# Kernel tuning notes

Hardware: AMD Instinct MI355X
Metric: run time of the kernel (lower is better)

Reference implementation:

```python
import jax, jax.numpy as jnp
import numpy as np
from jax import lax

T = 4          # num_steps
TAU = 2.0      # spikingjelly LIFNode default tau
VTH = 1.0      # v_threshold
ALPHA = 2.0    # ATan surrogate default alpha
EPS = 1e-5     # BatchNorm eps

@jax.custom_vjp
def atan_spike(x):
    # Heaviside forward, ATan surrogate backward (spikingjelly surrogate.ATan)
    return (x >= 0.0).astype(x.dtype)

def _atan_fwd(x):
    return atan_spike(x), x

def _atan_bwd(x, g):
    sg = (ALPHA / 2.0) / (1.0 + (jnp.pi / 2.0 * ALPHA * x) ** 2)
    return (g * sg,)

atan_spike.defvjp(_atan_fwd, _atan_bwd)

def lif_multistep(x_seq):
    # x_seq: (T, B, D, L). LIF with decay_input=True, v_reset=0.0, hard reset,
    # detach_reset=True (reset spike is stop-gradiented).
    def step(v, xt):
        h = v + (xt - v) / TAU          # membrane charge
        s = atan_spike(h - VTH)          # spike
        v_new = h * (1.0 - lax.stop_gradient(s))  # hard reset to 0
        return v_new, s
    _, spikes = lax.scan(step, jnp.zeros_like(x_seq[0]), x_seq)
    return spikes  # (T, B, D, L)

def setup_inputs() -> dict:
    key = jax.random.key(0)
    k1, k2, k3, k4 = jax.random.split(key, 4)
    L, TB, D = 2048, 128, 128
    x = jax.random.normal(k1, (L, TB, D), dtype=jnp.float32)
    conv_w = jax.random.normal(k2, (D, D, 3), dtype=jnp.float32) * 0.05
    bn_gamma = jnp.ones((D,), jnp.float32)
    bn_beta = jnp.zeros((D,), jnp.float32)
    bn_mean = jax.random.normal(k3, (D,), dtype=jnp.float32) * 0.1
    bn_var = jax.random.uniform(k4, (D,), dtype=jnp.float32, minval=0.5, maxval=1.5)
    return {"x": x, "conv_w": conv_w, "bn_gamma": bn_gamma, "bn_beta": bn_beta,
            "bn_mean": bn_mean, "bn_var": bn_var}

def reference(x, conv_w, bn_gamma, bn_beta, bn_mean, bn_var):
    # x: (L, TB, D)
    L, TB, D = x.shape
    xf = jnp.transpose(x, (1, 2, 0))  # (TB, D, L)
    # Conv1d(D, D, k=3, stride=1, pad=1, bias=False)
    xf = lax.conv_general_dilated(xf, conv_w, window_strides=(1,),
                                  padding=((1, 1),),
                                  dimension_numbers=("NCH", "OIH", "NCH"))
    # BatchNorm1d in inference mode (running stats)
    scale = bn_gamma * lax.rsqrt(bn_var + EPS)
    xf = (xf - bn_mean[None, :, None]) * scale[None, :, None] + bn_beta[None, :, None]
    # (TB, D, L) -> (T, B, D, L), multi-step LIF
    xs = xf.reshape(T, TB // T, D, L)
    sp = lif_multistep(xs)
    sp = sp.reshape(TB, D, L)   # flatten(0, 1); dropout is identity in eval
    return x + jnp.transpose(sp, (2, 0, 1))  # (L, TB, D)
```

## Files before the change

### kernel.cpp

```cpp
#include <hip/hip_runtime.h>


constexpr int L   = 2048;
constexpr int NTB = 128;
constexpr int D   = 128;
constexpr int T   = 4;
constexpr int LT  = 64;
constexpr int NP  = LT + 2;
constexpr int JT  = 16;
constexpr int IT  = 8;
constexpr int WROW = 52;

__global__ __launch_bounds__(256, 3)
void snn_conv_lif(const float* __restrict__ x, const float* __restrict__ w,
                  const float* __restrict__ gamma, const float* __restrict__ beta,
                  const float* __restrict__ mean, const float* __restrict__ var,
                  float* __restrict__ out) {
    __shared__ float xs[NP * D];
    __shared__ float ws[64 * WROW];

    const int tid = threadIdx.x;
    const int b   = blockIdx.x & 31;
    const int lt  = blockIdx.x >> 5;
    const int l0  = lt * LT;
    const int q   = tid & 63;
    const int lh  = tid >> 6;
    const int p0  = lh * JT;

    const int o0 = 2 * q, o1 = o0 + 1;
    const float sc0 = gamma[o0] / sqrtf(var[o0] + 1e-5f);
    const float bi0 = beta[o0] - mean[o0] * sc0;
    const float sc1 = gamma[o1] / sqrtf(var[o1] + 1e-5f);
    const float bi1 = beta[o1] - mean[o1] * sc1;

    float v0[JT], v1[JT];
    #pragma unroll
    for (int j = 0; j < JT; ++j) { v0[j] = 0.f; v1[j] = 0.f; }

    #pragma unroll 1
    for (int t = 0; t < T; ++t) {
        const int n = t * 32 + b;
        __syncthreads();
        for (int idx = tid; idx < NP * 32; idx += 256) {
            const int p = idx >> 5, c = idx & 31;
            const int l = l0 - 1 + p;
            float4 val = make_float4(0.f, 0.f, 0.f, 0.f);
            if (l >= 0 && l < L)
                val = ((const float4*)x)[l * (NTB * D / 4) + n * (D / 4) + c];
            ((float4*)xs)[p * (D / 4) + c] = val;
        }

        float a0[JT], a1[JT];
        #pragma unroll
        for (int j = 0; j < JT; ++j) { a0[j] = 0.f; a1[j] = 0.f; }

        #pragma unroll 1
        for (int it = 0; it < D / IT; ++it) {
            __syncthreads();
            for (int idx = tid; idx < 768; idx += 256) {
                const int qq = idx / 12;
                const int r  = idx - qq * 12;
                const int oo = (r >= 6) ? 1 : 0;
                const int c  = r - 6 * oo;
                float4 wv = ((const float4*)(w + (2 * qq + oo) * (D * 3) + it * (IT * 3)))[c];
                *((float4*)(ws + qq * WROW + oo * 28 + c * 4)) = wv;
            }
            __syncthreads();

            const float* wrow = ws + q * WROW;
            #pragma unroll
            for (int i4 = 0; i4 < IT / 4; ++i4) {
                const float4 wa0 = *((const float4*)(wrow + i4 * 12));
                const float4 wa1 = *((const float4*)(wrow + i4 * 12 + 4));
                const float4 wa2 = *((const float4*)(wrow + i4 * 12 + 8));
                const float4 wb0 = *((const float4*)(wrow + 28 + i4 * 12));
                const float4 wb1 = *((const float4*)(wrow + 28 + i4 * 12 + 4));
                const float4 wb2 = *((const float4*)(wrow + 28 + i4 * 12 + 8));
                const float wA[12] = {wa0.x, wa0.y, wa0.z, wa0.w,
                                      wa1.x, wa1.y, wa1.z, wa1.w,
                                      wa2.x, wa2.y, wa2.z, wa2.w};
                const float wB[12] = {wb0.x, wb0.y, wb0.z, wb0.w,
                                      wb1.x, wb1.y, wb1.z, wb1.w,
                                      wb2.x, wb2.y, wb2.z, wb2.w};
                const float4* xcol = (const float4*)xs + (it * 2 + i4);
                float4 xa = xcol[(p0 + 0) * (D / 4)];
                float4 xb = xcol[(p0 + 1) * (D / 4)];
                #pragma unroll
                for (int j = 0; j < JT; ++j) {
                    const float4 xc = xcol[(p0 + j + 2) * (D / 4)];
                    float s0 = a0[j];
                    float s1 = a1[j];
                    s0 = fmaf(xa.x, wA[0], s0);   s1 = fmaf(xa.x, wB[0], s1);
                    s0 = fmaf(xa.y, wA[3], s0);   s1 = fmaf(xa.y, wB[3], s1);
                    s0 = fmaf(xa.z, wA[6], s0);   s1 = fmaf(xa.z, wB[6], s1);
                    s0 = fmaf(xa.w, wA[9], s0);   s1 = fmaf(xa.w, wB[9], s1);
                    s0 = fmaf(xb.x, wA[1], s0);   s1 = fmaf(xb.x, wB[1], s1);
                    s0 = fmaf(xb.y, wA[4], s0);   s1 = fmaf(xb.y, wB[4], s1);
                    s0 = fmaf(xb.z, wA[7], s0);   s1 = fmaf(xb.z, wB[7], s1);
                    s0 = fmaf(xb.w, wA[10], s0);  s1 = fmaf(xb.w, wB[10], s1);
                    s0 = fmaf(xc.x, wA[2], s0);   s1 = fmaf(xc.x, wB[2], s1);
                    s0 = fmaf(xc.y, wA[5], s0);   s1 = fmaf(xc.y, wB[5], s1);
                    s0 = fmaf(xc.z, wA[8], s0);   s1 = fmaf(xc.z, wB[8], s1);
                    s0 = fmaf(xc.w, wA[11], s0);  s1 = fmaf(xc.w, wB[11], s1);
                    a0[j] = s0; a1[j] = s1;
                    xa = xb; xb = xc;
                }
            }
        }

        #pragma unroll
        for (int j = 0; j < JT; ++j) {
            const float y0 = fmaf(a0[j], sc0, bi0);
            const float y1 = fmaf(a1[j], sc1, bi1);
            const float h0 = 0.5f * (v0[j] + y0);
            const float h1 = 0.5f * (v1[j] + y1);
            const bool f0 = (h0 >= 1.0f);
            const bool f1 = (h1 >= 1.0f);
            v0[j] = f0 ? 0.0f : h0;
            v1[j] = f1 ? 0.0f : h1;
            const int l = l0 + p0 + j;
            const float2 res = ((const float2*)xs)[(p0 + j + 1) * (D / 2) + q];
            float2 ov;
            ov.x = res.x + (f0 ? 1.0f : 0.0f);
            ov.y = res.y + (f1 ? 1.0f : 0.0f);
            ((float2*)out)[(l * NTB + n) * (D / 2) + q] = ov;
        }
    }
}

extern "C" void kernel_launch(void* const* d_in, const int* in_sizes, int n_in,
                              void* d_out, int out_size, void* d_ws, size_t ws_size,
                              hipStream_t stream) {
    const float* x     = (const float*)d_in[0];
    const float* w     = (const float*)d_in[1];
    const float* gamma = (const float*)d_in[2];
    const float* beta  = (const float*)d_in[3];
    const float* mean  = (const float*)d_in[4];
    const float* var   = (const float*)d_in[5];
    float* out = (float*)d_out;

    dim3 grid((L / LT) * 32);
    dim3 block(256);
    snn_conv_lif<<<grid, block, 0, stream>>>(x, w, gamma, beta, mean, var, out);
}
```

Measured before the change: 623.2 us.

## Read conv inputs directly from global and double-buffer weight tiles in LDS

Drops the shared-memory staging of the input tile. Each wave now loads its x values straight from global memory as wave-uniform broadcast loads, since lh is made uniform with readfirstlane. Weight chunks are double-buffered in LDS, with the next chunk prefetched into registers while the current one is used, so each inner iteration needs one barrier instead of two. The trade-off is many more global/L1 loads for x in place of LDS reads, and it relies on scalar or broadcast loads being cheap.

```diff
diff --git a/kernel.cpp b/kernel.cpp
--- a/kernel.cpp
+++ b/kernel.cpp
@@ -6,32 +6,50 @@
 constexpr int D   = 128;
 constexpr int T   = 4;
 constexpr int LT  = 64;
-constexpr int NP  = LT + 2;
 constexpr int JT  = 16;
 constexpr int IT  = 8;
 constexpr int WROW = 52;
+
+__device__ __forceinline__ float4 ldx(const float* __restrict__ x, int l, int n, int cb) {
+    const int lc = (l < 0) ? 0 : ((l >= L) ? (L - 1) : l);
+    float4 v = ((const float4*)x)[(lc * NTB + n) * (D / 4) + cb];
+    if (l < 0 || l >= L) v = make_float4(0.f, 0.f, 0.f, 0.f);
+    return v;
+}
 
 __global__ __launch_bounds__(256, 3)
 void snn_conv_lif(const float* __restrict__ x, const float* __restrict__ w,
                   const float* __restrict__ gamma, const float* __restrict__ beta,
                   const float* __restrict__ mean, const float* __restrict__ var,
                   float* __restrict__ out) {
-    __shared__ float xs[NP * D];
-    __shared__ float ws[64 * WROW];
+    __shared__ float ws[2][64 * WROW];
 
     const int tid = threadIdx.x;
     const int b   = blockIdx.x & 31;
     const int lt  = blockIdx.x >> 5;
     const int l0  = lt * LT;
     const int q   = tid & 63;
-    const int lh  = tid >> 6;
+    const int lh  = __builtin_amdgcn_readfirstlane(tid >> 6);
     const int p0  = lh * JT;
+    const int lb  = l0 - 1 + p0;
 
     const int o0 = 2 * q, o1 = o0 + 1;
     const float sc0 = gamma[o0] / sqrtf(var[o0] + 1e-5f);
     const float bi0 = beta[o0] - mean[o0] * sc0;
     const float sc1 = gamma[o1] / sqrtf(var[o1] + 1e-5f);
     const float bi1 = beta[o1] - mean[o1] * sc1;
+
+    const int qq = tid >> 2;
+    const int r3 = 3 * (tid & 3);
+    int grow[3], lrow[3];
+    #pragma unroll
+    for (int c = 0; c < 3; ++c) {
+        const int rr = r3 + c;
+        const int oo = (rr >= 6) ? 1 : 0;
+        const int c6 = rr - 6 * oo;
+        grow[c] = (2 * qq + oo) * (D * 3) + c6 * 4;
+        lrow[c] = qq * WROW + oo * 28 + c6 * 4;
+    }
 
     float v0[JT], v1[JT];
     #pragma unroll
@@ -40,15 +58,13 @@
     #pragma unroll 1
     for (int t = 0; t < T; ++t) {
         const int n = t * 32 + b;
+
+        #pragma unroll
+        for (int c = 0; c < 3; ++c) {
+            const float4 wv = *((const float4*)(w + grow[c]));
+            *((float4*)(&ws[0][lrow[c]])) = wv;
+        }
         __syncthreads();
-        for (int idx = tid; idx < NP * 32; idx += 256) {
-            const int p = idx >> 5, c = idx & 31;
-            const int l = l0 - 1 + p;
-            float4 val = make_float4(0.f, 0.f, 0.f, 0.f);
-            if (l >= 0 && l < L)
-                val = ((const float4*)x)[l * (NTB * D / 4) + n * (D / 4) + c];
-            ((float4*)xs)[p * (D / 4) + c] = val;
-        }
 
         float a0[JT], a1[JT];
         #pragma unroll
@@ -56,18 +72,16 @@
 
         #pragma unroll 1
         for (int it = 0; it < D / IT; ++it) {
-            __syncthreads();
-            for (int idx = tid; idx < 768; idx += 256) {
-                const int qq = idx / 12;
-                const int r  = idx - qq * 12;
-                const int oo = (r >= 6) ? 1 : 0;
-                const int c  = r - 6 * oo;
-                float4 wv = ((const float4*)(w + (2 * qq + oo) * (D * 3) + it * (IT * 3)))[c];
-                *((float4*)(ws + qq * WROW + oo * 28 + c * 4)) = wv;
+            const int cur = it & 1;
+
+            float4 wp[3];
+            if (it < 15) {
+                #pragma unroll
+                for (int c = 0; c < 3; ++c)
+                    wp[c] = *((const float4*)(w + grow[c] + (it + 1) * (IT * 3)));
             }
-            __syncthreads();
 
-            const float* wrow = ws + q * WROW;
+            const float* wrow = &ws[cur][q * WROW];
             #pragma unroll
             for (int i4 = 0; i4 < IT / 4; ++i4) {
                 const float4 wa0 = *((const float4*)(wrow + i4 * 12));
@@ -82,12 +96,13 @@
                 const float wB[12] = {wb0.x, wb0.y, wb0.z, wb0.w,
                                       wb1.x, wb1.y, wb1.z, wb1.w,
                                       wb2.x, wb2.y, wb2.z, wb2.w};
-                const float4* xcol = (const float4*)xs + (it * 2 + i4);
-                float4 xa = xcol[(p0 + 0) * (D / 4)];
-                float4 xb = xcol[(p0 + 1) * (D / 4)];
+
+                const int cb = it * 2 + i4;
+                float4 xa = ldx(x, lb + 0, n, cb);
+                float4 xb = ldx(x, lb + 1, n, cb);
                 #pragma unroll
                 for (int j = 0; j < JT; ++j) {
-                    const float4 xc = xcol[(p0 + j + 2) * (D / 4)];
+                    const float4 xc = ldx(x, lb + j + 2, n, cb);
                     float s0 = a0[j];
                     float s1 = a1[j];
                     s0 = fmaf(xa.x, wA[0], s0);   s1 = fmaf(xa.x, wB[0], s1);
@@ -106,6 +121,13 @@
                     xa = xb; xb = xc;
                 }
             }
+
+            if (it < 15) {
+                #pragma unroll
+                for (int c = 0; c < 3; ++c)
+                    *((float4*)(&ws[cur ^ 1][lrow[c]])) = wp[c];
+            }
+            __syncthreads();
         }
 
         #pragma unroll
@@ -119,7 +141,7 @@
             v0[j] = f0 ? 0.0f : h0;
             v1[j] = f1 ? 0.0f : h1;
             const int l = l0 + p0 + j;
-            const float2 res = ((const float2*)xs)[(p0 + j + 1) * (D / 2) + q];
+            const float2 res = ((const float2*)x)[(l * NTB + n) * (D / 2) + q];
             float2 ov;
             ov.x = res.x + (f0 ? 1.0f : 0.0f);
             ov.y = res.y + (f1 ? 1.0f : 0.0f);
```

Result: slower. 1.844 ms (+195.8%).

## Load conv weights directly from global into registers with software prefetch

Applied to the files above, without the earlier changes.

Drops the shared-memory weight staging and its two barriers per 8-channel chunk. Each thread now reads its two output channels' weight rows straight from global memory (L1/L2 cached) into registers, prefetching the next 4-channel group while computing the current one. This removes LDS traffic and the frequent __syncthreads. The cost is more vector registers and uncoalesced global loads, since each lane reads a different 1.5KB row.

```diff
diff --git a/kernel.cpp b/kernel.cpp
--- a/kernel.cpp
+++ b/kernel.cpp
@@ -8,8 +8,6 @@
 constexpr int LT  = 64;
 constexpr int NP  = LT + 2;
 constexpr int JT  = 16;
-constexpr int IT  = 8;
-constexpr int WROW = 52;
 
 __global__ __launch_bounds__(256, 3)
 void snn_conv_lif(const float* __restrict__ x, const float* __restrict__ w,
@@ -17,7 +15,6 @@
                   const float* __restrict__ mean, const float* __restrict__ var,
                   float* __restrict__ out) {
     __shared__ float xs[NP * D];
-    __shared__ float ws[64 * WROW];
 
     const int tid = threadIdx.x;
     const int b   = blockIdx.x & 31;
@@ -33,6 +30,9 @@
     const float sc1 = gamma[o1] / sqrtf(var[o1] + 1e-5f);
     const float bi1 = beta[o1] - mean[o1] * sc1;
 
+    const float* w0 = w + o0 * (D * 3);
+    const float* w1 = w + o1 * (D * 3);
+
     float v0[JT], v1[JT];
     #pragma unroll
     for (int j = 0; j < JT; ++j) { v0[j] = 0.f; v1[j] = 0.f; }
@@ -46,7 +46,7 @@
             const int l = l0 - 1 + p;
             float4 val = make_float4(0.f, 0.f, 0.f, 0.f);
             if (l >= 0 && l < L)
-                val = ((const float4*)x)[l * (NTB * D / 4) + n * (D / 4) + c];
+                val = ((const float4*)x)[(l * NTB + n) * (D / 4) + c];
             ((float4*)xs)[p * (D / 4) + c] = val;
         }
 
@@ -54,58 +54,61 @@
         #pragma unroll
         for (int j = 0; j < JT; ++j) { a0[j] = 0.f; a1[j] = 0.f; }
 
-        #pragma unroll 1
-        for (int it = 0; it < D / IT; ++it) {
-            __syncthreads();
-            for (int idx = tid; idx < 768; idx += 256) {
-                const int qq = idx / 12;
-                const int r  = idx - qq * 12;
-                const int oo = (r >= 6) ? 1 : 0;
-                const int c  = r - 6 * oo;
-                float4 wv = ((const float4*)(w + (2 * qq + oo) * (D * 3) + it * (IT * 3)))[c];
-                *((float4*)(ws + qq * WROW + oo * 28 + c * 4)) = wv;
+        float4 wcA0 = *((const float4*)(w0 + 0));
+        float4 wcA1 = *((const float4*)(w0 + 4));
+        float4 wcA2 = *((const float4*)(w0 + 8));
+        float4 wcB0 = *((const float4*)(w1 + 0));
+        float4 wcB1 = *((const float4*)(w1 + 4));
+        float4 wcB2 = *((const float4*)(w1 + 8));
+        __syncthreads();
+
+        #pragma unroll 2
+        for (int ii = 0; ii < 32; ++ii) {
+            float4 wnA0, wnA1, wnA2, wnB0, wnB1, wnB2;
+            if (ii < 31) {
+                const float* pa = w0 + (ii + 1) * 12;
+                const float* pb = w1 + (ii + 1) * 12;
+                wnA0 = *((const float4*)(pa));
+                wnA1 = *((const float4*)(pa + 4));
+                wnA2 = *((const float4*)(pa + 8));
+                wnB0 = *((const float4*)(pb));
+                wnB1 = *((const float4*)(pb + 4));
+                wnB2 = *((const float4*)(pb + 8));
             }
-            __syncthreads();
 
-            const float* wrow = ws + q * WROW;
+            const float wA[12] = {wcA0.x, wcA0.y, wcA0.z, wcA0.w,
+                                  wcA1.x, wcA1.y, wcA1.z, wcA1.w,
+                                  wcA2.x, wcA2.y, wcA2.z, wcA2.w};
+            const float wB[12] = {wcB0.x, wcB0.y, wcB0.z, wcB0.w,
+                                  wcB1.x, wcB1.y, wcB1.z, wcB1.w,
+                                  wcB2.x, wcB2.y, wcB2.z, wcB2.w};
+
+            const float4* xcol = (const float4*)xs + ii;
+            float4 xa = xcol[(p0 + 0) * (D / 4)];
+            float4 xb = xcol[(p0 + 1) * (D / 4)];
             #pragma unroll
-            for (int i4 = 0; i4 < IT / 4; ++i4) {
-                const float4 wa0 = *((const float4*)(wrow + i4 * 12));
-                const float4 wa1 = *((const float4*)(wrow + i4 * 12 + 4));
-                const float4 wa2 = *((const float4*)(wrow + i4 * 12 + 8));
-                const float4 wb0 = *((const float4*)(wrow + 28 + i4 * 12));
-                const float4 wb1 = *((const float4*)(wrow + 28 + i4 * 12 + 4));
-                const float4 wb2 = *((const float4*)(wrow + 28 + i4 * 12 + 8));
-                const float wA[12] = {wa0.x, wa0.y, wa0.z, wa0.w,
-                                      wa1.x, wa1.y, wa1.z, wa1.w,
-                                      wa2.x, wa2.y, wa2.z, wa2.w};
-                const float wB[12] = {wb0.x, wb0.y, wb0.z, wb0.w,
-                                      wb1.x, wb1.y, wb1.z, wb1.w,
-                                      wb2.x, wb2.y, wb2.z, wb2.w};
-                const float4* xcol = (const float4*)xs + (it * 2 + i4);
-                float4 xa = xcol[(p0 + 0) * (D / 4)];
-                float4 xb = xcol[(p0 + 1) * (D / 4)];
-                #pragma unroll
-                for (int j = 0; j < JT; ++j) {
-                    const float4 xc = xcol[(p0 + j + 2) * (D / 4)];
-                    float s0 = a0[j];
-                    float s1 = a1[j];
-                    s0 = fmaf(xa.x, wA[0], s0);   s1 = fmaf(xa.x, wB[0], s1);
-                    s0 = fmaf(xa.y, wA[3], s0);   s1 = fmaf(xa.y, wB[3], s1);
-                    s0 = fmaf(xa.z, wA[6], s0);   s1 = fmaf(xa.z, wB[6], s1);
-                    s0 = fmaf(xa.w, wA[9], s0);   s1 = fmaf(xa.w, wB[9], s1);
-                    s0 = fmaf(xb.x, wA[1], s0);   s1 = fmaf(xb.x, wB[1], s1);
-                    s0 = fmaf(xb.y, wA[4], s0);   s1 = fmaf(xb.y, wB[4], s1);
-                    s0 = fmaf(xb.z, wA[7], s0);   s1 = fmaf(xb.z, wB[7], s1);
-                    s0 = fmaf(xb.w, wA[10], s0);  s1 = fmaf(xb.w, wB[10], s1);
-                    s0 = fmaf(xc.x, wA[2], s0);   s1 = fmaf(xc.x, wB[2], s1);
-                    s0 = fmaf(xc.y, wA[5], s0);   s1 = fmaf(xc.y, wB[5], s1);
-                    s0 = fmaf(xc.z, wA[8], s0);   s1 = fmaf(xc.z, wB[8], s1);
-                    s0 = fmaf(xc.w, wA[11], s0);  s1 = fmaf(xc.w, wB[11], s1);
-                    a0[j] = s0; a1[j] = s1;
-                    xa = xb; xb = xc;
-                }
+            for (int j = 0; j < JT; ++j) {
+                const float4 xc = xcol[(p0 + j + 2) * (D / 4)];
+                float s0 = a0[j];
+                float s1 = a1[j];
+                s0 = fmaf(xa.x, wA[0], s0);   s1 = fmaf(xa.x, wB[0], s1);
+                s0 = fmaf(xa.y, wA[3], s0);   s1 = fmaf(xa.y, wB[3], s1);
+                s0 = fmaf(xa.z, wA[6], s0);   s1 = fmaf(xa.z, wB[6], s1);
+                s0 = fmaf(xa.w, wA[9], s0);   s1 = fmaf(xa.w, wB[9], s1);
+                s0 = fmaf(xb.x, wA[1], s0);   s1 = fmaf(xb.x, wB[1], s1);
+                s0 = fmaf(xb.y, wA[4], s0);   s1 = fmaf(xb.y, wB[4], s1);
+                s0 = fmaf(xb.z, wA[7], s0);   s1 = fmaf(xb.z, wB[7], s1);
+                s0 = fmaf(xb.w, wA[10], s0);  s1 = fmaf(xb.w, wB[10], s1);
+                s0 = fmaf(xc.x, wA[2], s0);   s1 = fmaf(xc.x, wB[2], s1);
+                s0 = fmaf(xc.y, wA[5], s0);   s1 = fmaf(xc.y, wB[5], s1);
+                s0 = fmaf(xc.z, wA[8], s0);   s1 = fmaf(xc.z, wB[8], s1);
+                s0 = fmaf(xc.w, wA[11], s0);  s1 = fmaf(xc.w, wB[11], s1);
+                a0[j] = s0; a1[j] = s1;
+                xa = xb; xb = xc;
             }
+
+            wcA0 = wnA0; wcA1 = wnA1; wcA2 = wnA2;
+            wcB0 = wnB0; wcB1 = wnB1; wcB2 = wnB2;
         }
 
         #pragma unroll
```

Result: slower. 1.110 ms (+78.2%).
